# Kernel optimization log

Measured on AMD Instinct MI355X. Metric: run time of the kernel, lower is better.

The kernel has to match this reference:

```python
import jax, jax.numpy as jnp
import numpy as np
import math

D_MODEL = 1024
N_HEADS = 16
D_K = D_MODEL // N_HEADS
WIDTH_MULTIPLIER = 1.0  # readout=False on all projections, so unused in math


def setup_inputs() -> dict:
    key = jax.random.key(0)
    kx, kq, kk, kv, ko = jax.random.split(key, 5)
    std = 1.0 / math.sqrt(D_MODEL)  # init_scale=1.0 / sqrt(in_features)
    x = jax.random.normal(kx, (2, 2048, D_MODEL), dtype=jnp.float32)
    # weights stored as (out_features, in_features), matching torch
    Wq = jax.random.normal(kq, (D_MODEL, D_MODEL), dtype=jnp.float32) * std
    Wk = jax.random.normal(kk, (D_MODEL, D_MODEL), dtype=jnp.float32) * std
    Wv = jax.random.normal(kv, (D_MODEL, D_MODEL), dtype=jnp.float32) * std
    Wo = jax.random.normal(ko, (D_MODEL, D_MODEL), dtype=jnp.float32) * std
    return {"x": x, "Wq": Wq, "Wk": Wk, "Wv": Wv, "Wo": Wo}


def reference(x, Wq, Wk, Wv, Wo):
    B, S, D = x.shape
    H, Dk = N_HEADS, D_K
    # muPLinear: x @ W.T (bias=False, readout=False)
    q = jnp.einsum('bsd,ed->bse', x, Wq).reshape(B, S, H, Dk).transpose(0, 2, 1, 3)
    k = jnp.einsum('bsd,ed->bse', x, Wk).reshape(B, S, H, Dk).transpose(0, 2, 1, 3)
    v = jnp.einsum('bsd,ed->bse', x, Wv).reshape(B, S, H, Dk).transpose(0, 2, 1, 3)
    # full [B,H,S,S] scores, scaled by 1/sqrt(d_k), softmax over keys
    scores = jnp.einsum('bhqd,bhkd->bhqk', q, k) / math.sqrt(Dk)
    attn = jax.nn.softmax(scores, axis=-1)
    out = jnp.einsum('bhqk,bhkd->bhqd', attn, v)
    out = out.transpose(0, 2, 1, 3).reshape(B, S, D)
    return jnp.einsum('bsd,ed->bse', out, Wo)
```

## Files before the change

### kernel.cpp

```cpp
#include <hip/hip_runtime.h>
#include <hip/hip_bf16.h>
#include <math.h>

#define D_MODEL 1024
#define N_HEADS 16
#define D_K     64
#define BATCH   2
#define SEQ     2048
#define M_TOTAL (BATCH * SEQ)

typedef __attribute__((ext_vector_type(8))) short short8;
typedef __attribute__((ext_vector_type(2))) float f32x2;
typedef __attribute__((ext_vector_type(4))) float f32x4;
typedef __attribute__((ext_vector_type(16))) float f32x16;

__device__ __forceinline__ ushort f2bf(float f) {
    __hip_bfloat16 h = __float2bfloat16(f);
    union { __hip_bfloat16 h; ushort u; } c; c.h = h; return c.u;
}

__device__ __forceinline__ uint cvtpk(float a, float b) {
    uint r;
    asm("v_cvt_pk_bf16_f32 %0, %1, %2" : "=v"(r) : "v"(a), "v"(b));
    return r;
}

__device__ __forceinline__ f32x2 pk_mul(f32x2 a, f32x2 b) {
    f32x2 d;
    asm("v_pk_mul_f32 %0, %1, %2" : "=v"(d) : "v"(a), "v"(b));
    return d;
}
__device__ __forceinline__ f32x2 pk_add(f32x2 a, f32x2 b) {
    f32x2 d;
    asm("v_pk_add_f32 %0, %1, %2" : "=v"(d) : "v"(a), "v"(b));
    return d;
}
__device__ __forceinline__ float max3f(float a, float b, float c) {
    float d;
    asm("v_max3_f32 %0, %1, %2, %3" : "=v"(d) : "v"(a), "v"(b), "v"(c));
    return d;
}

__device__ __forceinline__ void gload_lds16(const void* g, void* l) {
    __builtin_amdgcn_global_load_lds(
        (const __attribute__((address_space(1))) void*)g,
        (__attribute__((address_space(3))) void*)l, 16, 0, 0);
}

__device__ __forceinline__ void plswap(uint& a, uint& b) {
    asm volatile("v_permlane32_swap_b32 %0, %1" : "+v"(a), "+v"(b));
}

__global__ __launch_bounds__(256) void cast_all(const float* __restrict__ x,
                                                const float* __restrict__ Wq,
                                                const float* __restrict__ Wk,
                                                const float* __restrict__ Wv,
                                                const float* __restrict__ Wo,
                                                ushort* __restrict__ xb,
                                                ushort* __restrict__ wqkv,
                                                ushort* __restrict__ wob)
{
    const int bi = blockIdx.x;
    const float* src; ushort* dst; int blk;
    const int NW = D_MODEL * D_MODEL;
    if (bi < 4096)      { src = x;  dst = xb;            blk = bi; }
    else if (bi < 5120) { src = Wq; dst = wqkv;          blk = bi - 4096; }
    else if (bi < 6144) { src = Wk; dst = wqkv + NW;     blk = bi - 5120; }
    else if (bi < 7168) { src = Wv; dst = wqkv + 2 * NW; blk = bi - 6144; }
    else                { src = Wo; dst = wob;           blk = bi - 7168; }
    const int i = blk * 1024 + threadIdx.x * 4;
    float4 v = *(const float4*)&src[i];
    ushort4 o;
    o.x = f2bf(v.x); o.y = f2bf(v.y); o.z = f2bf(v.z); o.w = f2bf(v.w);
    *(ushort4*)&dst[i] = o;
}

template <int EPI>
__global__ __launch_bounds__(256) void gemm_bf16(const ushort* __restrict__ A,
                                                 const ushort* __restrict__ B,
                                                 void* __restrict__ C0,
                                                 void* __restrict__ C1,
                                                 void* __restrict__ C2,
                                                 int M, int N, int K)
{
    __shared__ ushort As[2][4 * 128 * 8];
    __shared__ ushort Bs[2][4 * 128 * 8];

    const int tid = threadIdx.x;
    const int lane = tid & 63;
    const int w = tid >> 6;
    const int li = lane & 15;
    const int kg = lane >> 4;
    const int m0 = blockIdx.y * 128;
    const int n0 = blockIdx.x * 128;
    const int wr = (w >> 1) * 64;
    const int wc = (w & 1) * 64;

    f32x4 acc[4][4] = {};

    const int s1 = tid, s2 = tid + 256;
    const ushort* ga1 = &A[(size_t)(m0 + (s1 & 127)) * K + (s1 >> 7) * 8];
    const ushort* ga2 = &A[(size_t)(m0 + (s2 & 127)) * K + (s2 >> 7) * 8];
    const ushort* gb1 = &B[(size_t)(n0 + (s1 & 127)) * K + (s1 >> 7) * 8];
    const ushort* gb2 = &B[(size_t)(n0 + (s2 & 127)) * K + (s2 >> 7) * 8];

    const int NT = K / 32;
    gload_lds16(ga1, &As[0][s1 * 8]);
    gload_lds16(ga2, &As[0][s2 * 8]);
    gload_lds16(gb1, &Bs[0][s1 * 8]);
    gload_lds16(gb2, &Bs[0][s2 * 8]);

    for (int t = 0; t < NT; ++t) {
        const int cur = t & 1;
        asm volatile("s_waitcnt vmcnt(0)" ::: "memory");
        __syncthreads();
        if (t + 1 < NT) {
            const int kb = (t + 1) * 32;
            const int nxt = cur ^ 1;
            gload_lds16(ga1 + kb, &As[nxt][s1 * 8]);
            gload_lds16(ga2 + kb, &As[nxt][s2 * 8]);
            gload_lds16(gb1 + kb, &Bs[nxt][s1 * 8]);
            gload_lds16(gb2 + kb, &Bs[nxt][s2 * 8]);
        }
        short8 af[4], bf_[4];
#pragma unroll
        for (int m = 0; m < 4; ++m)
            af[m] = *(const short8*)&As[cur][(kg * 128 + wr + m * 16 + li) * 8];
#pragma unroll
        for (int n = 0; n < 4; ++n)
            bf_[n] = *(const short8*)&Bs[cur][(kg * 128 + wc + n * 16 + li) * 8];
#pragma unroll
        for (int m = 0; m < 4; ++m)
#pragma unroll
            for (int n = 0; n < 4; ++n)
                acc[m][n] = __builtin_amdgcn_mfma_f32_16x16x32_bf16(
                    af[m], bf_[n], acc[m][n], 0, 0, 0);
    }

    if (EPI == 1) {
        ushort* q = (ushort*)C0; ushort* k = (ushort*)C1; ushort* v = (ushort*)C2;
        const float QSCALE = 0.125f * 1.44269504088896f;
#pragma unroll
        for (int m = 0; m < 4; ++m) {
            const int Rb = m0 + wr + m * 16 + kg * 4;
#pragma unroll
            for (int n = 0; n < 4; ++n) {
                const int Ncol = n0 + wc + n * 16 + li;
                const int proj = Ncol >> 10;
                const int rem = Ncol & 1023;
                const int h = rem >> 6, dk = rem & 63;
#pragma unroll
                for (int r = 0; r < 4; ++r) {
                    const int R = Rb + r;
                    const int b = R >> 11, s = R & 2047;
                    const int bh = b * N_HEADS + h;
                    if (proj == 0)
                        q[((size_t)bh * SEQ + s) * D_K + dk] = f2bf(acc[m][n][r] * QSCALE);
                    else if (proj == 1)
                        k[((size_t)bh * SEQ + s) * D_K + dk] = f2bf(acc[m][n][r]);
                    else
                        v[((size_t)bh * D_K + dk) * SEQ + s] = f2bf(acc[m][n][r]);
                }
            }
        }
    } else {
        float* C = (float*)C0;
#pragma unroll
        for (int m = 0; m < 4; ++m) {
            const int Rb = m0 + wr + m * 16 + kg * 4;
#pragma unroll
            for (int n = 0; n < 4; ++n) {
                const int Ncol = n0 + wc + n * 16 + li;
#pragma unroll
                for (int r = 0; r < 4; ++r)
                    C[(size_t)(Rb + r) * N + Ncol] = acc[m][n][r];
            }
        }
    }
}

__global__ __launch_bounds__(512, 4) void attn_mfma(const ushort* __restrict__ Q,
                                                    const ushort* __restrict__ K,
                                                    const ushort* __restrict__ Vt,
                                                    ushort* __restrict__ AO)
{
    __shared__ ushort pool[2][2][2][64 * 64];

    const int tid = threadIdx.x, lane = tid & 63, w = tid >> 6;
    const int wq = w & 3, kvh = w >> 2;
    const int r31 = lane & 31, hi = lane >> 5;
    const int b = blockIdx.z, h = blockIdx.y, q0 = blockIdx.x * 128;
    const int bh = b * N_HEADS + h;
    const size_t base = (size_t)bh * SEQ * D_K;
    const size_t vbase = (size_t)bh * D_K * SEQ;

    uint pa = (uint)lane, pbv = 1000u + (uint)lane;
    plswap(pa, pbv);
    const bool swap_lo = (__builtin_amdgcn_readfirstlane(pa) > 500u);

    const size_t qrow = base + (size_t)(q0 + wq * 32 + r31) * D_K;
    short8 qb[4];
#pragma unroll
    for (int ks = 0; ks < 4; ++ks)
        qb[ks] = *(const short8*)&Q[qrow + ks * 16 + hi * 8];

    float m_ = -INFINITY, l_ = 0.f;
    f32x2 cpair = {0.f, 0.f};
    f32x16 o0 = {}, o1 = {};

    const int srow_l = lane >> 3;
    const int sblk = lane & 7;
    const ushort* Kt0 = &K[base];
    const ushort* Vt0 = &Vt[vbase];
    const int tile0 = kvh * 16;

    const int xr = r31 & 7;
    int off[2][4];
#pragma unroll
    for (int hf = 0; hf < 2; ++hf)
#pragma unroll
        for (int ks = 0; ks < 4; ++ks)
            off[hf][ks] = hf * 2048 + r31 * 64 + (((2 * ks + hi) ^ xr) * 8);

    const ushort* Kst = &pool[kvh][0][0][0];
    const ushort* Vst = &pool[kvh][1][0][0];

#define STAGE(kt_, buf_)                                                       \
    {                                                                          \
        _Pragma("unroll")                                                      \
        for (int p = 0; p < 2; ++p) {                                          \
            const int row = wq * 16 + p * 8 + srow_l;                          \
            const int db = sblk ^ (row & 7);                                   \
            gload_lds16(Kt0 + ((size_t)((tile0 + (kt_)) * 64 + row)) * D_K + db * 8, \
                        &pool[kvh][0][buf_][(wq * 16 + p * 8) * 64]);          \
            gload_lds16(Vt0 + (size_t)row * SEQ + (tile0 + (kt_)) * 64 + db * 8,     \
                        &pool[kvh][1][buf_][(wq * 16 + p * 8) * 64]);          \
        }                                                                      \
    }

    STAGE(0, 0);

    const int NT = SEQ / 64 / 2;
    for (int kt = 0; kt < NT; ++kt) {
        const int cur = kt & 1;
        asm volatile("s_waitcnt vmcnt(0)" ::: "memory");
        __syncthreads();
        if (kt + 1 < NT) STAGE(kt + 1, cur ^ 1);
        const ushort* Kc = Kst + cur * 4096;
        const ushort* Vc = Vst + cur * 4096;

#pragma unroll
        for (int hh = 0; hh < 2; ++hh) {
            f32x16 s = {};
            __builtin_amdgcn_s_setprio(1);
#pragma unroll
            for (int ks = 0; ks < 4; ++ks) {
                short8 kb = *(const short8*)(Kc + off[hh][ks]);
                s = __builtin_amdgcn_mfma_f32_32x32x16_bf16(kb, qb[ks], s, 0, 0, 0);
            }
            __builtin_amdgcn_s_setprio(0);

            float t0 = max3f(s[0], s[1], s[2]);
            float t1 = max3f(s[3], s[4], s[5]);
            float t2 = max3f(s[6], s[7], s[8]);
            float t3 = max3f(s[9], s[10], s[11]);
            float t4 = max3f(s[12], s[13], s[14]);
            t0 = max3f(t0, t1, s[15]);
            t2 = max3f(t2, t3, t4);
            float mx = fmaxf(t0, t2);
            mx = fmaxf(mx, __shfl_xor(mx, 32, 64));

            if (__any(mx > m_ + 8.0f)) {
                const float mn = fmaxf(m_, mx);
                const float sc = exp2f(m_ - mn);
                l_ *= sc;
#pragma unroll
                for (int e = 0; e < 16; ++e) { o0[e] *= sc; o1[e] *= sc; }
                m_ = mn;
                const float c = exp2f(-m_);
                cpair.x = c; cpair.y = c;
            }

            f32x2 ts0 = {0.f, 0.f};
            uint u[4][2];
#pragma unroll
            for (int rq = 0; rq < 4; ++rq) {
                f32x2 ea = {exp2f(s[4 * rq + 0]), exp2f(s[4 * rq + 1])};
                f32x2 eb = {exp2f(s[4 * rq + 2]), exp2f(s[4 * rq + 3])};
                f32x2 pa_ = pk_mul(ea, cpair);
                f32x2 pb_ = pk_mul(eb, cpair);
                ts0 = pk_add(ts0, pk_add(pa_, pb_));
                u[rq][0] = cvtpk(pa_.x, pa_.y);
                u[rq][1] = cvtpk(pb_.x, pb_.y);
            }
            float ts = ts0.x + ts0.y;
            ts += __shfl_xor(ts, 32, 64);
            l_ += ts;

            short8 pb[2];
#pragma unroll
            for (int ks = 0; ks < 2; ++ks) {
                uint x0 = u[2 * ks][0], x1 = u[2 * ks][1];
                uint y0 = u[2 * ks + 1][0], y1 = u[2 * ks + 1][1];
                if (swap_lo) { plswap(y0, x0); plswap(y1, x1); }
                else         { plswap(x0, y0); plswap(x1, y1); }
                union { uint u4[4]; short8 s; } pu;
                pu.u4[0] = x0; pu.u4[1] = x1; pu.u4[2] = y0; pu.u4[3] = y1;
                pb[ks] = pu.s;
            }

            __builtin_amdgcn_s_setprio(1);
#pragma unroll
            for (int ks = 0; ks < 2; ++ks) {
                short8 vb0 = *(const short8*)(Vc + off[0][2 * hh + ks]);
                short8 vb1 = *(const short8*)(Vc + off[1][2 * hh + ks]);
                o0 = __builtin_amdgcn_mfma_f32_32x32x16_bf16(vb0, pb[ks], o0, 0, 0, 0);
                o1 = __builtin_amdgcn_mfma_f32_32x32x16_bf16(vb1, pb[ks], o1, 0, 0, 0);
            }
            __builtin_amdgcn_s_setprio(0);
        }
    }
#undef STAGE

    __syncthreads();
    float* cs = (float*)&pool[0][0][0][0];
    float* ml = cs + 4 * 64 * 32;
    const int cidx = (wq * 64 + lane) * 32;
    if (kvh == 1) {
#pragma unroll
        for (int rq = 0; rq < 4; ++rq) {
            f32x4 a, c;
#pragma unroll
            for (int e = 0; e < 4; ++e) { a[e] = o0[4 * rq + e]; c[e] = o1[4 * rq + e]; }
            *(f32x4*)&cs[cidx + 4 * rq] = a;
            *(f32x4*)&cs[cidx + 16 + 4 * rq] = c;
        }
        ml[(wq * 64 + lane) * 2]     = m_;
        ml[(wq * 64 + lane) * 2 + 1] = l_;
    }
    __syncthreads();
    if (kvh == 0) {
        const float m2 = ml[(wq * 64 + lane) * 2];
        const float l2 = ml[(wq * 64 + lane) * 2 + 1];
        const float mM = fmaxf(m_, m2);
        const float sc1 = exp2f(m_ - mM), sc2 = exp2f(m2 - mM);
        const float linv = 1.f / (l_ * sc1 + l2 * sc2);
        ushort* Ao = &AO[((size_t)b * SEQ + q0 + wq * 32 + r31) * D_MODEL + h * 64];
#pragma unroll
        for (int rq = 0; rq < 4; ++rq) {
            f32x4 a = *(const f32x4*)&cs[cidx + 4 * rq];
            f32x4 c = *(const f32x4*)&cs[cidx + 16 + 4 * rq];
            uint2 v0, v1;
            v0.x = cvtpk((o0[4 * rq + 0] * sc1 + a[0] * sc2) * linv,
                         (o0[4 * rq + 1] * sc1 + a[1] * sc2) * linv);
            v0.y = cvtpk((o0[4 * rq + 2] * sc1 + a[2] * sc2) * linv,
                         (o0[4 * rq + 3] * sc1 + a[3] * sc2) * linv);
            v1.x = cvtpk((o1[4 * rq + 0] * sc1 + c[0] * sc2) * linv,
                         (o1[4 * rq + 1] * sc1 + c[1] * sc2) * linv);
            v1.y = cvtpk((o1[4 * rq + 2] * sc1 + c[2] * sc2) * linv,
                         (o1[4 * rq + 3] * sc1 + c[3] * sc2) * linv);
            *(uint2*)&Ao[8 * rq + 4 * hi]      = v0;
            *(uint2*)&Ao[32 + 8 * rq + 4 * hi] = v1;
        }
    }
}

extern "C" void kernel_launch(void* const* d_in, const int* in_sizes, int n_in,
                              void* d_out, int out_size, void* d_ws, size_t ws_size,
                              hipStream_t stream)
{
    const float* x  = (const float*)d_in[0];
    const float* Wq = (const float*)d_in[1];
    const float* Wk = (const float*)d_in[2];
    const float* Wv = (const float*)d_in[3];
    const float* Wo = (const float*)d_in[4];
    float* out = (float*)d_out;

    ushort* xb   = (ushort*)d_ws;
    ushort* Wqkv = xb + (size_t)M_TOTAL * D_MODEL;
    ushort* Wob  = Wqkv + (size_t)3 * D_MODEL * D_MODEL;
    ushort* q    = Wob + (size_t)D_MODEL * D_MODEL;
    ushort* k    = q + (size_t)M_TOTAL * D_MODEL;
    ushort* vt   = k + (size_t)M_TOTAL * D_MODEL;
    ushort* ao   = vt + (size_t)M_TOTAL * D_MODEL;

    hipLaunchKernelGGL(cast_all, dim3(8192), dim3(256), 0, stream,
                       x, Wq, Wk, Wv, Wo, xb, Wqkv, Wob);

    hipLaunchKernelGGL((gemm_bf16<1>), dim3(3 * D_MODEL / 128, M_TOTAL / 128), dim3(256),
                       0, stream, xb, Wqkv, q, k, vt, M_TOTAL, 3 * D_MODEL, D_MODEL);

    hipLaunchKernelGGL(attn_mfma, dim3(SEQ / 128, N_HEADS, BATCH), dim3(512),
                       0, stream, q, k, vt, ao);

    hipLaunchKernelGGL((gemm_bf16<0>), dim3(D_MODEL / 128, M_TOTAL / 128), dim3(256),
                       0, stream, ao, Wob, out, (void*)0, (void*)0,
                       M_TOTAL, D_MODEL, D_MODEL);
}
```

Before: 172.2 us.

## Load K/V fragments directly from global memory instead of LDS staging

Drops the double-buffered LDS staging of K and V tiles along with its per-tile barrier and waitcnt. Each wave now reads its MFMA K and V operand fragments straight from global memory, relying on L1/L2 caching since the four query waves read the same tiles. This removes synchronisation and LDS traffic. In exchange, global load latency is exposed inside the loop with no software prefetch, and the same data is fetched redundantly by every wave.

```diff
diff --git a/kernel.cpp b/kernel.cpp
--- a/kernel.cpp
+++ b/kernel.cpp
@@ -184,7 +184,7 @@
                                                     const ushort* __restrict__ Vt,
                                                     ushort* __restrict__ AO)
 {
-    __shared__ ushort pool[2][2][2][64 * 64];
+    __shared__ float cs[4 * 64 * 32 + 512];
 
     const int tid = threadIdx.x, lane = tid & 63, w = tid >> 6;
     const int wq = w & 3, kvh = w >> 2;
@@ -208,56 +208,36 @@
     f32x2 cpair = {0.f, 0.f};
     f32x16 o0 = {}, o1 = {};
 
-    const int srow_l = lane >> 3;
-    const int sblk = lane & 7;
-    const ushort* Kt0 = &K[base];
-    const ushort* Vt0 = &Vt[vbase];
     const int tile0 = kvh * 16;
-
-    const int xr = r31 & 7;
-    int off[2][4];
-#pragma unroll
-    for (int hf = 0; hf < 2; ++hf)
-#pragma unroll
-        for (int ks = 0; ks < 4; ++ks)
-            off[hf][ks] = hf * 2048 + r31 * 64 + (((2 * ks + hi) ^ xr) * 8);
-
-    const ushort* Kst = &pool[kvh][0][0][0];
-    const ushort* Vst = &pool[kvh][1][0][0];
-
-#define STAGE(kt_, buf_)                                                       \
-    {                                                                          \
-        _Pragma("unroll")                                                      \
-        for (int p = 0; p < 2; ++p) {                                          \
-            const int row = wq * 16 + p * 8 + srow_l;                          \
-            const int db = sblk ^ (row & 7);                                   \
-            gload_lds16(Kt0 + ((size_t)((tile0 + (kt_)) * 64 + row)) * D_K + db * 8, \
-                        &pool[kvh][0][buf_][(wq * 16 + p * 8) * 64]);          \
-            gload_lds16(Vt0 + (size_t)row * SEQ + (tile0 + (kt_)) * 64 + db * 8,     \
-                        &pool[kvh][1][buf_][(wq * 16 + p * 8) * 64]);          \
-        }                                                                      \
-    }
-
-    STAGE(0, 0);
+    const ushort* kgrp = K + base + (size_t)tile0 * 64 * D_K + r31 * 64 + hi * 8;
+    const ushort* vgrp = Vt + vbase + (size_t)tile0 * 64 + (size_t)r31 * SEQ + hi * 8;
 
     const int NT = SEQ / 64 / 2;
     for (int kt = 0; kt < NT; ++kt) {
-        const int cur = kt & 1;
-        asm volatile("s_waitcnt vmcnt(0)" ::: "memory");
-        __syncthreads();
-        if (kt + 1 < NT) STAGE(kt + 1, cur ^ 1);
-        const ushort* Kc = Kst + cur * 4096;
-        const ushort* Vc = Vst + cur * 4096;
+        const ushort* kp_t = kgrp + kt * 4096;
+        const ushort* vp_t = vgrp + kt * 64;
 
 #pragma unroll
         for (int hh = 0; hh < 2; ++hh) {
+            const ushort* kp = kp_t + hh * 2048;
+            const ushort* vp0 = vp_t + hh * 32;
+            const ushort* vp1 = vp0 + 32 * SEQ;
+
+            short8 kf0 = *(const short8*)(kp);
+            short8 kf1 = *(const short8*)(kp + 16);
+            short8 kf2 = *(const short8*)(kp + 32);
+            short8 kf3 = *(const short8*)(kp + 48);
+            short8 vf00 = *(const short8*)(vp0);
+            short8 vf01 = *(const short8*)(vp0 + 16);
+            short8 vf10 = *(const short8*)(vp1);
+            short8 vf11 = *(const short8*)(vp1 + 16);
+
             f32x16 s = {};
             __builtin_amdgcn_s_setprio(1);
-#pragma unroll
-            for (int ks = 0; ks < 4; ++ks) {
-                short8 kb = *(const short8*)(Kc + off[hh][ks]);
-                s = __builtin_amdgcn_mfma_f32_32x32x16_bf16(kb, qb[ks], s, 0, 0, 0);
-            }
+            s = __builtin_amdgcn_mfma_f32_32x32x16_bf16(kf0, qb[0], s, 0, 0, 0);
+            s = __builtin_amdgcn_mfma_f32_32x32x16_bf16(kf1, qb[1], s, 0, 0, 0);
+            s = __builtin_amdgcn_mfma_f32_32x32x16_bf16(kf2, qb[2], s, 0, 0, 0);
+            s = __builtin_amdgcn_mfma_f32_32x32x16_bf16(kf3, qb[3], s, 0, 0, 0);
             __builtin_amdgcn_s_setprio(0);
 
             float t0 = max3f(s[0], s[1], s[2]);
@@ -310,20 +290,15 @@
             }
 
             __builtin_amdgcn_s_setprio(1);
-#pragma unroll
-            for (int ks = 0; ks < 2; ++ks) {
-                short8 vb0 = *(const short8*)(Vc + off[0][2 * hh + ks]);
-                short8 vb1 = *(const short8*)(Vc + off[1][2 * hh + ks]);
-                o0 = __builtin_amdgcn_mfma_f32_32x32x16_bf16(vb0, pb[ks], o0, 0, 0, 0);
-                o1 = __builtin_amdgcn_mfma_f32_32x32x16_bf16(vb1, pb[ks], o1, 0, 0, 0);
-            }
+            o0 = __builtin_amdgcn_mfma_f32_32x32x16_bf16(vf00, pb[0], o0, 0, 0, 0);
+            o0 = __builtin_amdgcn_mfma_f32_32x32x16_bf16(vf01, pb[1], o0, 0, 0, 0);
+            o1 = __builtin_amdgcn_mfma_f32_32x32x16_bf16(vf10, pb[0], o1, 0, 0, 0);
+            o1 = __builtin_amdgcn_mfma_f32_32x32x16_bf16(vf11, pb[1], o1, 0, 0, 0);
             __builtin_amdgcn_s_setprio(0);
         }
     }
-#undef STAGE
 
     __syncthreads();
-    float* cs = (float*)&pool[0][0][0][0];
     float* ml = cs + 4 * 64 * 32;
     const int cidx = (wq * 64 + lane) * 32;
     if (kvh == 1) {
```

Result: slower. 228.7 us (+32.8%).
